# Optimization experiments

Measured on AMD Instinct MI355X. Metric: run time of the kernel, lower is better.

The kernel has to match this reference:

```python
import jax, jax.numpy as jnp
import numpy as np
from jax import lax

B, S, T, V, E, H = 32, 128, 64, 32000, 512, 512
STEPS = T - 1


def gru_cell(x, h, Wih, Whh, bih, bhh):
    # PyTorch GRU cell: gates ordered (r, z, n)
    gi = x @ Wih.T + bih            # [B, 3H]
    gh = h @ Whh.T + bhh            # [B, 3H]
    ir, iz, inn = jnp.split(gi, 3, axis=-1)
    hr, hz, hn = jnp.split(gh, 3, axis=-1)
    r = jax.nn.sigmoid(ir + hr)
    z = jax.nn.sigmoid(iz + hz)
    n = jnp.tanh(inn + r * hn)
    return (1.0 - z) * n + z * h


def setup_inputs() -> dict:
    key = jax.random.key(0)
    ks = jax.random.split(key, 16)
    w = lambda k, shape: (jax.random.normal(k, shape, dtype=jnp.float32) * 0.05)
    src = jax.random.randint(ks[0], (B, S), 1, V)
    src_lengths = jax.random.randint(ks[1], (B,), 1, S + 1)
    tgt = jax.random.randint(ks[2], (B, T), 1, V)
    return {
        'src': src, 'src_lengths': src_lengths, 'tgt': tgt,
        # encoder
        'emb_enc': w(ks[3], (V, E)).at[0].set(0.0),   # padding_idx=0
        'Wih_e': w(ks[4], (3 * H, E)),
        'Whh_e': w(ks[5], (3 * H, H)),
        'bih_e': jnp.zeros((3 * H,), jnp.float32),
        'bhh_e': jnp.zeros((3 * H,), jnp.float32),
        # decoder
        'emb_dec': w(ks[6], (V, E)).at[0].set(0.0),
        'Wih_d': w(ks[7], (3 * H, E + H)),
        'Whh_d': w(ks[8], (3 * H, H)),
        'bih_d': jnp.zeros((3 * H,), jnp.float32),
        'bhh_d': jnp.zeros((3 * H,), jnp.float32),
        'Wc': w(ks[9], (H, 2 * H)),
        'bc': jnp.zeros((H,), jnp.float32),
        'Wo': w(ks[10], (V, H)),
        'bo': jnp.zeros((V,), jnp.float32),
    }


def _forward(src, src_lengths, tgt, emb_enc, Wih_e, Whh_e, bih_e, bhh_e,
             emb_dec, Wih_d, Whh_d, bih_d, bhh_d, Wc, bc, Wo, bo):
    # ---- encoder (packed-sequence semantics: state frozen / outputs zero past length) ----
    x = emb_enc[src]                                   # [B, S, E]
    xs = jnp.swapaxes(x, 0, 1)                         # [S, B, E]
    valid = jnp.arange(S)[:, None] < src_lengths[None, :]  # [S, B]
    h0 = jnp.zeros((src.shape[0], H), x.dtype)

    def enc_step(h, inp):
        xt, vt = inp
        hn = gru_cell(xt, h, Wih_e, Whh_e, bih_e, bhh_e)
        h = jnp.where(vt[:, None], hn, h)
        out = jnp.where(vt[:, None], hn, 0.0)
        return h, out

    h_enc, enc_outs = lax.scan(enc_step, h0, (xs, valid))
    enc_outs = jnp.swapaxes(enc_outs, 0, 1)            # [B, S, H]
    mask = jnp.arange(S)[None, :] < src_lengths[:, None]  # [B, S]

    # ---- decoder loop (teacher forcing ratio 1.0 -> input = tgt[:, t]) ----
    tokens = jnp.swapaxes(tgt[:, :STEPS], 0, 1)        # [STEPS, B]

    def dec_step(h, tok):
        e = emb_dec[tok]                               # [B, E]
        query = h                                      # hidden[-1], 1 layer
        scores = jnp.einsum('bsh,bh->bs', enc_outs, query)
        scores = jnp.where(mask, scores, -jnp.inf)
        aw = jax.nn.softmax(scores, axis=1)            # [B, S]
        ctx = jnp.einsum('bs,bsh->bh', aw, enc_outs)   # [B, H]
        rnn_in = jnp.concatenate([e, ctx], axis=-1)    # [B, E+H]
        hn = gru_cell(rnn_in, h, Wih_d, Whh_d, bih_d, bhh_d)
        cc = jnp.tanh(jnp.concatenate([hn, ctx], axis=-1) @ Wc.T + bc)
        logits = cc @ Wo.T + bo                        # [B, V]
        return hn, (logits, aw)

    _, (logits, attns) = lax.scan(dec_step, h_enc, tokens)
    logits = jnp.swapaxes(logits, 0, 1)                # [B, STEPS, V]
    attns = jnp.swapaxes(attns, 0, 1)                  # [B, STEPS, S]
    return logits, attns


def reference(src, src_lengths, tgt, emb_enc, Wih_e, Whh_e, bih_e, bhh_e,
              emb_dec, Wih_d, Whh_d, bih_d, bhh_d, Wc, bc, Wo, bo):
    return _forward(src, src_lengths, tgt, emb_enc, Wih_e, Whh_e, bih_e, bhh_e,
                    emb_dec, Wih_d, Whh_d, bih_d, bhh_d, Wc, bc, Wo, bo)
```

## Files before the change

### kernel.cpp

```cpp
#include <hip/hip_runtime.h>
#include <hip/hip_fp16.h>
#include <cmath>

#define B_ 32
#define S_ 128
#define T_ 64
#define STEPS_ 63
#define V_ 32000
#define E_ 512
#define H_ 512

typedef __attribute__((ext_vector_type(4))) float f32x4;
typedef __attribute__((ext_vector_type(8))) short bf16x8;
typedef __attribute__((ext_vector_type(2))) _Float16 f16x2;

__device__ inline short f2bf(float x) {
  unsigned u = __builtin_bit_cast(unsigned, x);
  u = (u + 0x7fffu + ((u >> 16) & 1u)) >> 16;
  return (short)u;
}
__device__ inline float bf2f(short h) {
  unsigned u = ((unsigned)(unsigned short)h) << 16;
  return __builtin_bit_cast(float, u);
}
__device__ inline float fdot2(__half2 a, __half2 b, float c) {
#if __has_builtin(__builtin_amdgcn_fdot2)
  return __builtin_amdgcn_fdot2(__builtin_bit_cast(f16x2, a),
                                __builtin_bit_cast(f16x2, b), c, false);
#else
  float2 af = __half22float2(a), bf = __half22float2(b);
  return c + af.x * bf.x + af.y * bf.y;
#endif
}
__device__ inline float sigm(float x) { return 1.f / (1.f + expf(-x)); }

__global__ __launch_bounds__(256) void k_pack_w3(
    const float* __restrict__ W, int ldw, int col0, __half* __restrict__ W3) {
  int idx = blockIdx.x * 256 + threadIdx.x;
  int up = idx & 255, g = (idx >> 8) % 3, kq = idx / 768;
  const float* r0 = W + (long)(g * 512 + 2 * up) * ldw + col0 + 4 * kq;
  const float* r1 = r0 + ldw;
  __half h[8];
  h[0] = __float2half(r0[0]); h[1] = __float2half(r0[1]);
  h[2] = __float2half(r1[0]); h[3] = __float2half(r1[1]);
  h[4] = __float2half(r0[2]); h[5] = __float2half(r0[3]);
  h[6] = __float2half(r1[2]); h[7] = __float2half(r1[3]);
  *(uint4*)(W3 + (long)idx * 8) = *(uint4*)h;
}

__global__ __launch_bounds__(256) void k_mfma_gemm(
    const float* __restrict__ A, const float* __restrict__ emb,
    const int* __restrict__ tok, int amode,
    const float* __restrict__ Bmat, long ldb,
    const float* __restrict__ bias,
    void* __restrict__ outp, long sb, long st,
    int M, int N, int K, int outmode, int passes) {
  __shared__ short Ah[128 * 40];
  __shared__ short Al[128 * 40];
  __shared__ short Bh[128 * 40];
  __shared__ short Bl[128 * 40];
  int t = threadIdx.x;
  int n0 = blockIdx.x * 128, m0 = blockIdx.y * 128;
  int ar = t >> 2, ac = (t & 3) * 8;

  const float* arow0;
  const float* arow1;
  {
    int m = m0 + ar;       int mc = m < M ? m : M - 1;
    int m2 = m0 + ar + 64; int mc2 = m2 < M ? m2 : M - 1;
    if (amode == 0) {
      arow0 = A + (long)mc * K;
      arow1 = A + (long)mc2 * K;
    } else {
      int b = mc & 31, q = mc >> 5;
      int tk = (amode == 1) ? tok[b * S_ + q] : tok[b * T_ + q];
      arow0 = emb + (long)tk * K;
      b = mc2 & 31; q = mc2 >> 5;
      tk = (amode == 1) ? tok[b * S_ + q] : tok[b * T_ + q];
      arow1 = emb + (long)tk * K;
    }
  }
  const float* brow0 = Bmat + (long)(n0 + ar) * ldb;
  const float* brow1 = Bmat + (long)(n0 + ar + 64) * ldb;

  int lane = t & 63, wave = t >> 6;
  int wm = (wave >> 1) * 64, wn = (wave & 1) * 64;
  int lr = lane & 15, lk = lane >> 4;
  f32x4 acc[4][4] = {};

  for (int k0 = 0; k0 < K; k0 += 32) {
    auto stage = [&](const float* rowp, short* Dh, short* Dl, int r) {
      float4 x0 = *(const float4*)(rowp + k0 + ac);
      float4 x1 = *(const float4*)(rowp + k0 + ac + 4);
      float xs[8] = {x0.x, x0.y, x0.z, x0.w, x1.x, x1.y, x1.z, x1.w};
      bf16x8 hi, lo;
#pragma unroll
      for (int i = 0; i < 8; ++i) {
        short h = f2bf(xs[i]);
        hi[i] = h;
        lo[i] = f2bf(xs[i] - bf2f(h));
      }
      *(bf16x8*)&Dh[r * 40 + ac] = hi;
      if (passes > 1) *(bf16x8*)&Dl[r * 40 + ac] = lo;
    };
    stage(arow0, Ah, Al, ar);
    stage(arow1, Ah, Al, ar + 64);
    stage(brow0, Bh, Bl, ar);
    stage(brow1, Bh, Bl, ar + 64);
    __syncthreads();

    bf16x8 a_h[4], b_h[4];
#pragma unroll
    for (int i = 0; i < 4; ++i) {
      a_h[i] = *(const bf16x8*)&Ah[(wm + i * 16 + lr) * 40 + lk * 8];
      b_h[i] = *(const bf16x8*)&Bh[(wn + i * 16 + lr) * 40 + lk * 8];
    }
    if (passes > 1) {
      bf16x8 a_l[4], b_l[4];
#pragma unroll
      for (int i = 0; i < 4; ++i) {
        a_l[i] = *(const bf16x8*)&Al[(wm + i * 16 + lr) * 40 + lk * 8];
        b_l[i] = *(const bf16x8*)&Bl[(wn + i * 16 + lr) * 40 + lk * 8];
      }
#pragma unroll
      for (int i = 0; i < 4; ++i)
#pragma unroll
        for (int j = 0; j < 4; ++j) {
          acc[i][j] = __builtin_amdgcn_mfma_f32_16x16x32_bf16(a_l[i], b_h[j], acc[i][j], 0, 0, 0);
          acc[i][j] = __builtin_amdgcn_mfma_f32_16x16x32_bf16(a_h[i], b_l[j], acc[i][j], 0, 0, 0);
        }
    }
#pragma unroll
    for (int i = 0; i < 4; ++i)
#pragma unroll
      for (int j = 0; j < 4; ++j)
        acc[i][j] = __builtin_amdgcn_mfma_f32_16x16x32_bf16(a_h[i], b_h[j], acc[i][j], 0, 0, 0);
    __syncthreads();
  }

#pragma unroll
  for (int i = 0; i < 4; ++i) {
#pragma unroll
    for (int r = 0; r < 4; ++r) {
      int m = m0 + wm + i * 16 + lk * 4 + r;
      if (m >= M) continue;
      long base = (long)(m & 31) * sb + (long)(m >> 5) * st;
#pragma unroll
      for (int j = 0; j < 4; ++j) {
        int n = n0 + wn + j * 16 + lr;
        float v = acc[i][j][r] + bias[n];
        if (outmode == 2) ((__half*)outp)[base + n] = __float2half(v);
        else ((float*)outp)[base + n] = (outmode == 1) ? tanhf(v) : v;
      }
    }
  }
}

__global__ __launch_bounds__(1024) void k_enc_all(
    const float* __restrict__ gi_all,
    const __half* __restrict__ W3,
    const float* __restrict__ bhh, const int* __restrict__ lens,
    float* __restrict__ h_out,
    __half* __restrict__ EO16,
    float* __restrict__ EO32) {
  __shared__ __align__(8) __half2 hs16[256];
  __shared__ float pGh[1536];
  __shared__ float gis[1536];
  int b = blockIdx.x, t = threadIdx.x;
  int len = lens[b];
  float br0 = 0, br1 = 0, bz0 = 0, bz1 = 0, bn0 = 0, bn1 = 0, hold0 = 0, hold1 = 0;
  if (t < 256) {
    br0 = bhh[2 * t]; br1 = bhh[2 * t + 1];
    bz0 = bhh[512 + 2 * t]; bz1 = bhh[512 + 2 * t + 1];
    bn0 = bhh[1024 + 2 * t]; bn1 = bhh[1024 + 2 * t + 1];
    hs16[t] = __float22half2_rn(make_float2(0.f, 0.f));
  }
  __syncthreads();

  for (int s = 0; s < S_; ++s) {
    if (s == len) break;
    if (t >= 256) {
      int c = t - 256, g = c >> 8, up = c & 255;
      const __half* wb = W3 + (long)(g * 256 + up) * 8;
      float a0 = 0.f, a1 = 0.f;
#pragma unroll 8
      for (int kq = 0; kq < 128; ++kq) {
        uint4 w8 = *(const uint4*)(wb + (long)kq * 6144);
        const __half2* wp = (const __half2*)&w8;
        __half2 x01 = hs16[2 * kq], x23 = hs16[2 * kq + 1];
        a0 = fdot2(x01, wp[0], a0); a1 = fdot2(x01, wp[1], a1);
        a0 = fdot2(x23, wp[2], a0); a1 = fdot2(x23, wp[3], a1);
      }
      pGh[g * 512 + 2 * up] = a0;
      pGh[g * 512 + 2 * up + 1] = a1;
    } else {
      const float* gi = gi_all + ((long)s * 32 + b) * 1536;
      int i0 = t * 6;
#pragma unroll
      for (int i = 0; i < 6; ++i) gis[i0 + i] = gi[i0 + i];
    }
    __syncthreads();
    if (t < 256) {
      int u0 = 2 * t;
      float r0 = sigm(gis[u0] + pGh[u0] + br0);
      float r1 = sigm(gis[u0 + 1] + pGh[u0 + 1] + br1);
      float z0 = sigm(gis[512 + u0] + pGh[512 + u0] + bz0);
      float z1 = sigm(gis[512 + u0 + 1] + pGh[512 + u0 + 1] + bz1);
      float n0 = tanhf(gis[1024 + u0] + r0 * (pGh[1024 + u0] + bn0));
      float n1 = tanhf(gis[1024 + u0 + 1] + r1 * (pGh[1024 + u0 + 1] + bn1));
      hold0 = (1.f - z0) * n0 + z0 * hold0;
      hold1 = (1.f - z1) * n1 + z1 * hold1;
      __half2 h2 = __float22half2_rn(make_float2(hold0, hold1));
      hs16[t] = h2;
      long row = (long)b * 128 + s;
      *(__half2*)(EO16 + row * 512 + u0) = h2;
      *(float2*)(EO32 + row * 512 + u0) = make_float2(hold0, hold1);
    }
    __syncthreads();
  }
  if (t < 256) *(float2*)(h_out + b * 512 + 2 * t) = make_float2(hold0, hold1);
}

__global__ __launch_bounds__(1024) void k_dec_all(
    const float* __restrict__ gie,
    const __half* __restrict__ EO16g,
    const __half* __restrict__ W3,
    const __half* __restrict__ GV,
    const float* __restrict__ bhh, const int* __restrict__ lens,
    const float* __restrict__ h_init,
    float* __restrict__ hctx,
    float* __restrict__ attns) {
  __shared__ __align__(16) __half2 EOs[32768];
  __shared__ __align__(8) __half2 hs16[256];
  __shared__ float pGh[1536];
  __shared__ float pGc[1536];
  __shared__ float gis[1536];
  __shared__ float sc[128];
  __shared__ float wred[8];
  int b = blockIdx.x, t = threadIdx.x;
  int lane = t & 63, wave = t >> 6;
  int len = lens[b];
  float br0 = 0, br1 = 0, bz0 = 0, bz1 = 0, bn0 = 0, bn1 = 0, hold0 = 0, hold1 = 0;
  if (t < 256) {
    br0 = bhh[2 * t]; br1 = bhh[2 * t + 1];
    bz0 = bhh[512 + 2 * t]; bz1 = bhh[512 + 2 * t + 1];
    bn0 = bhh[1024 + 2 * t]; bn1 = bhh[1024 + 2 * t + 1];
    float2 h2 = *(const float2*)(h_init + b * 512 + 2 * t);
    hold0 = h2.x; hold1 = h2.y;
    hs16[t] = __float22half2_rn(h2);
  }
  {
    const uint4* src = (const uint4*)(EO16g + (long)b * 128 * 512);
    uint4* dst = (uint4*)EOs;
    for (int i = t; i < 8192; i += 1024) dst[i] = src[i];
  }
  __syncthreads();
  const __half2* GVb = (const __half2*)GV + (long)b * 128 * 768;

  for (int step = 0; step < STEPS_; ++step) {
    long row = (long)step * 32 + b;
    {
      uint4 hv = ((const uint4*)hs16)[lane];
      const __half2* hp = (const __half2*)&hv;
#pragma unroll
      for (int si = 0; si < 8; ++si) {
        int s = wave * 8 + si;
        uint4 ev = ((const uint4*)&EOs[s * 256])[lane];
        const __half2* ep = (const __half2*)&ev;
        float p = 0.f;
#pragma unroll
        for (int q = 0; q < 4; ++q) p = fdot2(ep[q], hp[q], p);
#pragma unroll
        for (int off = 32; off > 0; off >>= 1) p += __shfl_down(p, off, 64);
        if (lane == 0) sc[s] = p;
      }
    }
    __syncthreads();
    if (t < 128) {
      float v = (t < len) ? sc[t] : -INFINITY;
      float wm = v;
#pragma unroll
      for (int off = 32; off > 0; off >>= 1) wm = fmaxf(wm, __shfl_down(wm, off, 64));
      if (lane == 0) wred[wave] = wm;
    } else if (t < 512) {
      const float* gi = gie + row * 1536;
      int i0 = (t - 128) * 4;
      *(float4*)(gis + i0) = *(const float4*)(gi + i0);
    }
    __syncthreads();
    if (t < 128) {
      float m = fmaxf(wred[0], wred[1]);
      float e = (t < len) ? expf(sc[t] - m) : 0.f;
      float es = e;
#pragma unroll
      for (int off = 32; off > 0; off >>= 1) es += __shfl_down(es, off, 64);
      if (lane == 0) wred[4 + wave] = es;
      __syncthreads();
      float aw = e / (wred[4] + wred[5]);
      sc[t] = aw;
      attns[((long)b * STEPS_ + step) * 128 + t] = aw;
    } else {
      __syncthreads();
    }
    __syncthreads();
    if (t < 768) {
      int g = t >> 8, up = t & 255;
      const __half* wb = W3 + (long)(g * 256 + up) * 8;
      float a0 = 0.f, a1 = 0.f;
#pragma unroll 8
      for (int kq = 0; kq < 128; ++kq) {
        uint4 w8 = *(const uint4*)(wb + (long)kq * 6144);
        const __half2* wp = (const __half2*)&w8;
        __half2 x01 = hs16[2 * kq], x23 = hs16[2 * kq + 1];
        a0 = fdot2(x01, wp[0], a0); a1 = fdot2(x01, wp[1], a1);
        a0 = fdot2(x23, wp[2], a0); a1 = fdot2(x23, wp[3], a1);
      }
      pGh[g * 512 + 2 * up] = a0;
      pGh[g * 512 + 2 * up + 1] = a1;
    } else if (t < 960) {
      int c4 = (t - 768) * 4;
      float ax0 = 0, ay0 = 0, ax1 = 0, ay1 = 0, ax2 = 0, ay2 = 0, ax3 = 0, ay3 = 0;
#pragma unroll 2
      for (int s = 0; s < 128; ++s) {
        if (s == len) break;
        float aw = sc[s];
        uint4 g4 = *(const uint4*)(GVb + (long)s * 768 + c4);
        const __half2* gp = (const __half2*)&g4;
        float2 f0 = __half22float2(gp[0]), f1 = __half22float2(gp[1]);
        float2 f2 = __half22float2(gp[2]), f3 = __half22float2(gp[3]);
        ax0 += aw * f0.x; ay0 += aw * f0.y;
        ax1 += aw * f1.x; ay1 += aw * f1.y;
        ax2 += aw * f2.x; ay2 += aw * f2.y;
        ax3 += aw * f3.x; ay3 += aw * f3.y;
      }
      pGc[2 * c4 + 0] = ax0; pGc[2 * c4 + 1] = ay0;
      pGc[2 * c4 + 2] = ax1; pGc[2 * c4 + 3] = ay1;
      pGc[2 * c4 + 4] = ax2; pGc[2 * c4 + 5] = ay2;
      pGc[2 * c4 + 6] = ax3; pGc[2 * c4 + 7] = ay3;
    } else {
      int ec = (t - 960) * 4;
      float ax0 = 0, ay0 = 0, ax1 = 0, ay1 = 0, ax2 = 0, ay2 = 0, ax3 = 0, ay3 = 0;
#pragma unroll 2
      for (int s = 0; s < 128; ++s) {
        if (s == len) break;
        float aw = sc[s];
        uint4 e4 = ((const uint4*)&EOs[s * 256])[t - 960];
        const __half2* ep = (const __half2*)&e4;
        float2 f0 = __half22float2(ep[0]), f1 = __half22float2(ep[1]);
        float2 f2 = __half22float2(ep[2]), f3 = __half22float2(ep[3]);
        ax0 += aw * f0.x; ay0 += aw * f0.y;
        ax1 += aw * f1.x; ay1 += aw * f1.y;
        ax2 += aw * f2.x; ay2 += aw * f2.y;
        ax3 += aw * f3.x; ay3 += aw * f3.y;
      }
      float* crow = hctx + row * 1024 + 512 + 2 * ec;
      *(float2*)(crow + 0) = make_float2(ax0, ay0);
      *(float2*)(crow + 2) = make_float2(ax1, ay1);
      *(float2*)(crow + 4) = make_float2(ax2, ay2);
      *(float2*)(crow + 6) = make_float2(ax3, ay3);
    }
    __syncthreads();
    if (t < 256) {
      int u0 = 2 * t;
      float r0 = sigm(gis[u0] + pGc[u0] + pGh[u0] + br0);
      float r1 = sigm(gis[u0 + 1] + pGc[u0 + 1] + pGh[u0 + 1] + br1);
      float z0 = sigm(gis[512 + u0] + pGc[512 + u0] + pGh[512 + u0] + bz0);
      float z1 = sigm(gis[512 + u0 + 1] + pGc[512 + u0 + 1] + pGh[512 + u0 + 1] + bz1);
      float n0 = tanhf(gis[1024 + u0] + pGc[1024 + u0] + r0 * (pGh[1024 + u0] + bn0));
      float n1 = tanhf(gis[1024 + u0 + 1] + pGc[1024 + u0 + 1] + r1 * (pGh[1024 + u0 + 1] + bn1));
      hold0 = (1.f - z0) * n0 + z0 * hold0;
      hold1 = (1.f - z1) * n1 + z1 * hold1;
      hs16[t] = __float22half2_rn(make_float2(hold0, hold1));
      *(float2*)(hctx + row * 1024 + u0) = make_float2(hold0, hold1);
    }
    __syncthreads();
  }
}

extern "C" void kernel_launch(void* const* d_in, const int* in_sizes, int n_in,
                              void* d_out, int out_size, void* d_ws, size_t ws_size,
                              hipStream_t stream) {
  (void)in_sizes; (void)n_in; (void)out_size; (void)ws_size;
  const int*   src   = (const int*)d_in[0];
  const int*   lens  = (const int*)d_in[1];
  const int*   tgt   = (const int*)d_in[2];
  const float* emb_e = (const float*)d_in[3];
  const float* Wih_e = (const float*)d_in[4];
  const float* Whh_e = (const float*)d_in[5];
  const float* bih_e = (const float*)d_in[6];
  const float* bhh_e = (const float*)d_in[7];
  const float* emb_d = (const float*)d_in[8];
  const float* Wih_d = (const float*)d_in[9];
  const float* Whh_d = (const float*)d_in[10];
  const float* bih_d = (const float*)d_in[11];
  const float* bhh_d = (const float*)d_in[12];
  const float* Wc    = (const float*)d_in[13];
  const float* bc    = (const float*)d_in[14];
  const float* Wo    = (const float*)d_in[15];
  const float* bo    = (const float*)d_in[16];

  float* logits = (float*)d_out;
  float* attns  = (float*)d_out + (long)B_ * STEPS_ * V_;

  float* w = (float*)d_ws;
  __half* W3e  = (__half*)w;
  __half* W3d  = (__half*)(w + 393216);
  float*  zb   = w + 786432;
  float*  GIe  = w + 788480;
  float*  GId  = GIe + 6291456;
  __half* EO16 = (__half*)(GId + 3145728);
  float*  EO32 = GId + 3145728 + 1048576;
  float*  h0   = EO32 + 2097152;
  __half* GV    = (__half*)GIe;
  float*  hctx  = GIe + 3145728;
  float*  ccall = GIe + 5242880;

  hipMemsetAsync(EO16, 0, 2097152 * sizeof(__half), stream);
  hipMemsetAsync(EO32, 0, 2097152 * sizeof(float), stream);
  hipMemsetAsync(zb, 0, 1536 * sizeof(float), stream);

  k_pack_w3<<<384, 256, 0, stream>>>(Whh_e, 512, 0, W3e);
  k_pack_w3<<<384, 256, 0, stream>>>(Whh_d, 512, 0, W3d);

  k_mfma_gemm<<<dim3(1536 / 128, 4096 / 128), 256, 0, stream>>>(
      nullptr, emb_e, src, 1, Wih_e, 512, bih_e, GIe, 1536L, 32L * 1536L,
      4096, 1536, 512, 0, 1);
  k_mfma_gemm<<<dim3(1536 / 128, (2016 + 127) / 128), 256, 0, stream>>>(
      nullptr, emb_d, tgt, 2, Wih_d, 1024, bih_d, GId, 1536L, 32L * 1536L,
      2016, 1536, 512, 0, 1);

  k_enc_all<<<32, 1024, 0, stream>>>(GIe, W3e, bhh_e, lens, h0, EO16, EO32);

  k_mfma_gemm<<<dim3(1536 / 128, 4096 / 128), 256, 0, stream>>>(
      EO32, nullptr, nullptr, 0, Wih_d + 512, 1024, zb, GV, 1536L, 49152L,
      4096, 1536, 512, 2, 3);

  k_dec_all<<<32, 1024, 0, stream>>>(GId, EO16, W3d, GV, bhh_d, lens, h0,
                                     hctx, attns);

  k_mfma_gemm<<<dim3(512 / 128, (2016 + 127) / 128), 256, 0, stream>>>(
      hctx, nullptr, nullptr, 0, Wc, 1024, bc, ccall, 512L, 16384L,
      2016, 512, 1024, 1, 3);

  k_mfma_gemm<<<dim3(V_ / 128, (2016 + 127) / 128), 256, 0, stream>>>(
      ccall, nullptr, nullptr, 0, Wo, 512, bo, logits,
      (long)STEPS_ * V_, (long)V_, 2016, 32000, 512, 0, 3);
}
```

Measured before the change: 3.426 ms.

## Keep recurrent Whh weights resident in registers across encoder and decoder steps

Repacks Whh so that each of the 1024 threads preloads 96 uint4 (all three gates for one hidden unit over half of K) into registers once, instead of re-reading the packed weights from global/L2 every time step. All threads now take part in the h@Whh matvec, with a pair shuffle to combine the two K halves, and the separate pGh shared buffer and one barrier per step are removed. The decoder softmax is collapsed into a single wave, and the context accumulation is split across more threads with narrower per-thread work. This needs about 384 VGPRs per thread for weights, so there is risk of spilling or of the register limit under launch_bounds(1024,4).

```diff
diff --git a/kernel.cpp b/kernel.cpp
--- a/kernel.cpp
+++ b/kernel.cpp
@@ -34,18 +34,16 @@
 }
 __device__ inline float sigm(float x) { return 1.f / (1.f + expf(-x)); }
 
-__global__ __launch_bounds__(256) void k_pack_w3(
-    const float* __restrict__ W, int ldw, int col0, __half* __restrict__ W3) {
+__global__ __launch_bounds__(256) void k_pack_w4(
+    const float* __restrict__ W, int ldw, int col0, uint4* __restrict__ W4) {
   int idx = blockIdx.x * 256 + threadIdx.x;
-  int up = idx & 255, g = (idx >> 8) % 3, kq = idx / 768;
-  const float* r0 = W + (long)(g * 512 + 2 * up) * ldw + col0 + 4 * kq;
-  const float* r1 = r0 + ldw;
+  int t = idx & 1023, i = idx >> 10;
+  int g = i >> 5, ii = i & 31, u = t >> 1, kh = t & 1;
+  const float* r = W + (long)(g * 512 + u) * ldw + col0 + kh * 256 + ii * 8;
   __half h[8];
-  h[0] = __float2half(r0[0]); h[1] = __float2half(r0[1]);
-  h[2] = __float2half(r1[0]); h[3] = __float2half(r1[1]);
-  h[4] = __float2half(r0[2]); h[5] = __float2half(r0[3]);
-  h[6] = __float2half(r1[2]); h[7] = __float2half(r1[3]);
-  *(uint4*)(W3 + (long)idx * 8) = *(uint4*)h;
+#pragma unroll
+  for (int j = 0; j < 8; ++j) h[j] = __float2half(r[j]);
+  W4[idx] = *(uint4*)h;
 }
 
 __global__ __launch_bounds__(256) void k_mfma_gemm(
@@ -156,98 +154,94 @@
   }
 }
 
-__global__ __launch_bounds__(1024) void k_enc_all(
+__global__ __launch_bounds__(1024, 4) void k_enc_all(
     const float* __restrict__ gi_all,
-    const __half* __restrict__ W3,
+    const uint4* __restrict__ W4,
     const float* __restrict__ bhh, const int* __restrict__ lens,
     float* __restrict__ h_out,
     __half* __restrict__ EO16,
     float* __restrict__ EO32) {
-  __shared__ __align__(8) __half2 hs16[256];
-  __shared__ float pGh[1536];
-  __shared__ float gis[1536];
+  __shared__ __align__(16) __half hs16[512];
   int b = blockIdx.x, t = threadIdx.x;
+  int u = t >> 1, kh = t & 1;
   int len = lens[b];
-  float br0 = 0, br1 = 0, bz0 = 0, bz1 = 0, bn0 = 0, bn1 = 0, hold0 = 0, hold1 = 0;
-  if (t < 256) {
-    br0 = bhh[2 * t]; br1 = bhh[2 * t + 1];
-    bz0 = bhh[512 + 2 * t]; bz1 = bhh[512 + 2 * t + 1];
-    bn0 = bhh[1024 + 2 * t]; bn1 = bhh[1024 + 2 * t + 1];
-    hs16[t] = __float22half2_rn(make_float2(0.f, 0.f));
-  }
+  uint4 wreg[96];
+#pragma unroll
+  for (int i = 0; i < 96; ++i) wreg[i] = W4[(long)i * 1024 + t];
+  float bhr = bhh[u], bhz = bhh[512 + u], bhn = bhh[1024 + u];
+  float hcur = 0.f;
+  if (kh == 0) hs16[u] = __float2half(0.f);
   __syncthreads();
 
   for (int s = 0; s < S_; ++s) {
     if (s == len) break;
-    if (t >= 256) {
-      int c = t - 256, g = c >> 8, up = c & 255;
-      const __half* wb = W3 + (long)(g * 256 + up) * 8;
-      float a0 = 0.f, a1 = 0.f;
-#pragma unroll 8
-      for (int kq = 0; kq < 128; ++kq) {
-        uint4 w8 = *(const uint4*)(wb + (long)kq * 6144);
-        const __half2* wp = (const __half2*)&w8;
-        __half2 x01 = hs16[2 * kq], x23 = hs16[2 * kq + 1];
-        a0 = fdot2(x01, wp[0], a0); a1 = fdot2(x01, wp[1], a1);
-        a0 = fdot2(x23, wp[2], a0); a1 = fdot2(x23, wp[3], a1);
-      }
-      pGh[g * 512 + 2 * up] = a0;
-      pGh[g * 512 + 2 * up + 1] = a1;
-    } else {
+    float gi_r = 0, gi_z = 0, gi_n = 0;
+    if (kh == 0) {
       const float* gi = gi_all + ((long)s * 32 + b) * 1536;
-      int i0 = t * 6;
-#pragma unroll
-      for (int i = 0; i < 6; ++i) gis[i0 + i] = gi[i0 + i];
-    }
-    __syncthreads();
-    if (t < 256) {
-      int u0 = 2 * t;
-      float r0 = sigm(gis[u0] + pGh[u0] + br0);
-      float r1 = sigm(gis[u0 + 1] + pGh[u0 + 1] + br1);
-      float z0 = sigm(gis[512 + u0] + pGh[512 + u0] + bz0);
-      float z1 = sigm(gis[512 + u0 + 1] + pGh[512 + u0 + 1] + bz1);
-      float n0 = tanhf(gis[1024 + u0] + r0 * (pGh[1024 + u0] + bn0));
-      float n1 = tanhf(gis[1024 + u0 + 1] + r1 * (pGh[1024 + u0 + 1] + bn1));
-      hold0 = (1.f - z0) * n0 + z0 * hold0;
-      hold1 = (1.f - z1) * n1 + z1 * hold1;
-      __half2 h2 = __float22half2_rn(make_float2(hold0, hold1));
-      hs16[t] = h2;
+      gi_r = gi[u]; gi_z = gi[512 + u]; gi_n = gi[1024 + u];
+    }
+    float ar = 0.f, az = 0.f, an = 0.f;
+    const uint4* xv4 = ((const uint4*)hs16) + kh * 32;
+#pragma unroll
+    for (int i = 0; i < 32; ++i) {
+      uint4 xv = xv4[i];
+      const __half2* xp = (const __half2*)&xv;
+      const __half2* wr = (const __half2*)&wreg[i];
+      const __half2* wz = (const __half2*)&wreg[32 + i];
+      const __half2* wn = (const __half2*)&wreg[64 + i];
+#pragma unroll
+      for (int q = 0; q < 4; ++q) {
+        ar = fdot2(xp[q], wr[q], ar);
+        az = fdot2(xp[q], wz[q], az);
+        an = fdot2(xp[q], wn[q], an);
+      }
+    }
+    ar += __shfl_xor(ar, 1, 64);
+    az += __shfl_xor(az, 1, 64);
+    an += __shfl_xor(an, 1, 64);
+    __syncthreads();
+    if (kh == 0) {
+      float r = sigm(gi_r + ar + bhr);
+      float z = sigm(gi_z + az + bhz);
+      float n = tanhf(gi_n + r * (an + bhn));
+      hcur = (1.f - z) * n + z * hcur;
+      __half hh = __float2half(hcur);
+      hs16[u] = hh;
       long row = (long)b * 128 + s;
-      *(__half2*)(EO16 + row * 512 + u0) = h2;
-      *(float2*)(EO32 + row * 512 + u0) = make_float2(hold0, hold1);
-    }
-    __syncthreads();
-  }
-  if (t < 256) *(float2*)(h_out + b * 512 + 2 * t) = make_float2(hold0, hold1);
-}
-
-__global__ __launch_bounds__(1024) void k_dec_all(
+      EO16[row * 512 + u] = hh;
+      EO32[row * 512 + u] = hcur;
+    }
+    __syncthreads();
+  }
+  if (kh == 0) h_out[b * 512 + u] = hcur;
+}
+
+__global__ __launch_bounds__(1024, 4) void k_dec_all(
     const float* __restrict__ gie,
     const __half* __restrict__ EO16g,
-    const __half* __restrict__ W3,
+    const uint4* __restrict__ W4,
     const __half* __restrict__ GV,
     const float* __restrict__ bhh, const int* __restrict__ lens,
     const float* __restrict__ h_init,
     float* __restrict__ hctx,
     float* __restrict__ attns) {
   __shared__ __align__(16) __half2 EOs[32768];
-  __shared__ __align__(8) __half2 hs16[256];
-  __shared__ float pGh[1536];
+  __shared__ __align__(16) __half hs16[512];
   __shared__ float pGc[1536];
   __shared__ float gis[1536];
   __shared__ float sc[128];
-  __shared__ float wred[8];
   int b = blockIdx.x, t = threadIdx.x;
   int lane = t & 63, wave = t >> 6;
+  int u = t >> 1, kh = t & 1;
   int len = lens[b];
-  float br0 = 0, br1 = 0, bz0 = 0, bz1 = 0, bn0 = 0, bn1 = 0, hold0 = 0, hold1 = 0;
-  if (t < 256) {
-    br0 = bhh[2 * t]; br1 = bhh[2 * t + 1];
-    bz0 = bhh[512 + 2 * t]; bz1 = bhh[512 + 2 * t + 1];
-    bn0 = bhh[1024 + 2 * t]; bn1 = bhh[1024 + 2 * t + 1];
-    float2 h2 = *(const float2*)(h_init + b * 512 + 2 * t);
-    hold0 = h2.x; hold1 = h2.y;
-    hs16[t] = __float22half2_rn(h2);
+  uint4 wreg[96];
+#pragma unroll
+  for (int i = 0; i < 96; ++i) wreg[i] = W4[(long)i * 1024 + t];
+  float bhr = bhh[u], bhz = bhh[512 + u], bhn = bhh[1024 + u];
+  float hcur = 0.f;
+  if (kh == 0) {
+    hcur = h_init[b * 512 + u];
+    hs16[u] = __float2half(hcur);
   }
   {
     const uint4* src = (const uint4*)(EO16g + (long)b * 128 * 512);
@@ -276,102 +270,81 @@
       }
     }
     __syncthreads();
-    if (t < 128) {
-      float v = (t < len) ? sc[t] : -INFINITY;
-      float wm = v;
-#pragma unroll
-      for (int off = 32; off > 0; off >>= 1) wm = fmaxf(wm, __shfl_down(wm, off, 64));
-      if (lane == 0) wred[wave] = wm;
-    } else if (t < 512) {
-      const float* gi = gie + row * 1536;
-      int i0 = (t - 128) * 4;
-      *(float4*)(gis + i0) = *(const float4*)(gi + i0);
-    }
-    __syncthreads();
-    if (t < 128) {
-      float m = fmaxf(wred[0], wred[1]);
-      float e = (t < len) ? expf(sc[t] - m) : 0.f;
-      float es = e;
-#pragma unroll
-      for (int off = 32; off > 0; off >>= 1) es += __shfl_down(es, off, 64);
-      if (lane == 0) wred[4 + wave] = es;
-      __syncthreads();
-      float aw = e / (wred[4] + wred[5]);
-      sc[t] = aw;
-      attns[((long)b * STEPS_ + step) * 128 + t] = aw;
-    } else {
-      __syncthreads();
+    if (t < 64) {
+      float p0 = sc[lane], p1 = sc[64 + lane];
+      bool v0 = lane < len, v1 = 64 + lane < len;
+      float m = fmaxf(v0 ? p0 : -INFINITY, v1 ? p1 : -INFINITY);
+#pragma unroll
+      for (int off = 32; off > 0; off >>= 1) m = fmaxf(m, __shfl_xor(m, off, 64));
+      float e0 = v0 ? expf(p0 - m) : 0.f;
+      float e1 = v1 ? expf(p1 - m) : 0.f;
+      float S = e0 + e1;
+#pragma unroll
+      for (int off = 32; off > 0; off >>= 1) S += __shfl_xor(S, off, 64);
+      float aw0 = e0 / S, aw1 = e1 / S;
+      sc[lane] = aw0;
+      sc[64 + lane] = aw1;
+      float* ap = attns + ((long)b * STEPS_ + step) * 128;
+      ap[lane] = aw0;
+      ap[64 + lane] = aw1;
+    } else if (t < 448) {
+      int i0 = (t - 64) * 4;
+      *(float4*)(gis + i0) = *(const float4*)(gie + row * 1536 + i0);
     }
     __syncthreads();
     if (t < 768) {
-      int g = t >> 8, up = t & 255;
-      const __half* wb = W3 + (long)(g * 256 + up) * 8;
-      float a0 = 0.f, a1 = 0.f;
-#pragma unroll 8
-      for (int kq = 0; kq < 128; ++kq) {
-        uint4 w8 = *(const uint4*)(wb + (long)kq * 6144);
-        const __half2* wp = (const __half2*)&w8;
-        __half2 x01 = hs16[2 * kq], x23 = hs16[2 * kq + 1];
-        a0 = fdot2(x01, wp[0], a0); a1 = fdot2(x01, wp[1], a1);
-        a0 = fdot2(x23, wp[2], a0); a1 = fdot2(x23, wp[3], a1);
-      }
-      pGh[g * 512 + 2 * up] = a0;
-      pGh[g * 512 + 2 * up + 1] = a1;
-    } else if (t < 960) {
-      int c4 = (t - 768) * 4;
-      float ax0 = 0, ay0 = 0, ax1 = 0, ay1 = 0, ax2 = 0, ay2 = 0, ax3 = 0, ay3 = 0;
-#pragma unroll 2
+      float ax = 0.f, ay = 0.f;
       for (int s = 0; s < 128; ++s) {
         if (s == len) break;
         float aw = sc[s];
-        uint4 g4 = *(const uint4*)(GVb + (long)s * 768 + c4);
-        const __half2* gp = (const __half2*)&g4;
-        float2 f0 = __half22float2(gp[0]), f1 = __half22float2(gp[1]);
-        float2 f2 = __half22float2(gp[2]), f3 = __half22float2(gp[3]);
-        ax0 += aw * f0.x; ay0 += aw * f0.y;
-        ax1 += aw * f1.x; ay1 += aw * f1.y;
-        ax2 += aw * f2.x; ay2 += aw * f2.y;
-        ax3 += aw * f3.x; ay3 += aw * f3.y;
-      }
-      pGc[2 * c4 + 0] = ax0; pGc[2 * c4 + 1] = ay0;
-      pGc[2 * c4 + 2] = ax1; pGc[2 * c4 + 3] = ay1;
-      pGc[2 * c4 + 4] = ax2; pGc[2 * c4 + 5] = ay2;
-      pGc[2 * c4 + 6] = ax3; pGc[2 * c4 + 7] = ay3;
+        float2 g2 = __half22float2(GVb[(long)s * 768 + t]);
+        ax += aw * g2.x;
+        ay += aw * g2.y;
+      }
+      pGc[2 * t] = ax;
+      pGc[2 * t + 1] = ay;
     } else {
-      int ec = (t - 960) * 4;
-      float ax0 = 0, ay0 = 0, ax1 = 0, ay1 = 0, ax2 = 0, ay2 = 0, ax3 = 0, ay3 = 0;
-#pragma unroll 2
+      int c = t - 768;
+      float ax = 0.f, ay = 0.f;
       for (int s = 0; s < 128; ++s) {
         if (s == len) break;
         float aw = sc[s];
-        uint4 e4 = ((const uint4*)&EOs[s * 256])[t - 960];
-        const __half2* ep = (const __half2*)&e4;
-        float2 f0 = __half22float2(ep[0]), f1 = __half22float2(ep[1]);
-        float2 f2 = __half22float2(ep[2]), f3 = __half22float2(ep[3]);
-        ax0 += aw * f0.x; ay0 += aw * f0.y;
-        ax1 += aw * f1.x; ay1 += aw * f1.y;
-        ax2 += aw * f2.x; ay2 += aw * f2.y;
-        ax3 += aw * f3.x; ay3 += aw * f3.y;
-      }
-      float* crow = hctx + row * 1024 + 512 + 2 * ec;
-      *(float2*)(crow + 0) = make_float2(ax0, ay0);
-      *(float2*)(crow + 2) = make_float2(ax1, ay1);
-      *(float2*)(crow + 4) = make_float2(ax2, ay2);
-      *(float2*)(crow + 6) = make_float2(ax3, ay3);
-    }
-    __syncthreads();
-    if (t < 256) {
-      int u0 = 2 * t;
-      float r0 = sigm(gis[u0] + pGc[u0] + pGh[u0] + br0);
-      float r1 = sigm(gis[u0 + 1] + pGc[u0 + 1] + pGh[u0 + 1] + br1);
-      float z0 = sigm(gis[512 + u0] + pGc[512 + u0] + pGh[512 + u0] + bz0);
-      float z1 = sigm(gis[512 + u0 + 1] + pGc[512 + u0 + 1] + pGh[512 + u0 + 1] + bz1);
-      float n0 = tanhf(gis[1024 + u0] + pGc[1024 + u0] + r0 * (pGh[1024 + u0] + bn0));
-      float n1 = tanhf(gis[1024 + u0 + 1] + pGc[1024 + u0 + 1] + r1 * (pGh[1024 + u0 + 1] + bn1));
-      hold0 = (1.f - z0) * n0 + z0 * hold0;
-      hold1 = (1.f - z1) * n1 + z1 * hold1;
-      hs16[t] = __float22half2_rn(make_float2(hold0, hold1));
-      *(float2*)(hctx + row * 1024 + u0) = make_float2(hold0, hold1);
+        float2 e2 = __half22float2(EOs[s * 256 + c]);
+        ax += aw * e2.x;
+        ay += aw * e2.y;
+      }
+      *(float2*)(hctx + row * 1024 + 512 + 2 * c) = make_float2(ax, ay);
+    }
+    __syncthreads();
+    float ar = 0.f, az = 0.f, an = 0.f;
+    {
+      const uint4* xv4 = ((const uint4*)hs16) + kh * 32;
+#pragma unroll
+      for (int i = 0; i < 32; ++i) {
+        uint4 xv = xv4[i];
+        const __half2* xp = (const __half2*)&xv;
+        const __half2* wr = (const __half2*)&wreg[i];
+        const __half2* wz = (const __half2*)&wreg[32 + i];
+        const __half2* wn = (const __half2*)&wreg[64 + i];
+#pragma unroll
+        for (int q = 0; q < 4; ++q) {
+          ar = fdot2(xp[q], wr[q], ar);
+          az = fdot2(xp[q], wz[q], az);
+          an = fdot2(xp[q], wn[q], an);
+        }
+      }
+      ar += __shfl_xor(ar, 1, 64);
+      az += __shfl_xor(az, 1, 64);
+      an += __shfl_xor(an, 1, 64);
+    }
+    __syncthreads();
+    if (kh == 0) {
+      float r = sigm(gis[u] + pGc[u] + ar + bhr);
+      float z = sigm(gis[512 + u] + pGc[512 + u] + az + bhz);
+      float n = tanhf(gis[1024 + u] + pGc[1024 + u] + r * (an + bhn));
+      hcur = (1.f - z) * n + z * hcur;
+      hs16[u] = __float2half(hcur);
+      hctx[row * 1024 + u] = hcur;
     }
     __syncthreads();
   }
@@ -403,8 +376,8 @@
   float* attns  = (float*)d_out + (long)B_ * STEPS_ * V_;
 
   float* w = (float*)d_ws;
-  __half* W3e  = (__half*)w;
-  __half* W3d  = (__half*)(w + 393216);
+  uint4*  W4e  = (uint4*)w;
+  uint4*  W4d  = (uint4*)(w + 393216);
   float*  zb   = w + 786432;
   float*  GIe  = w + 788480;
   float*  GId  = GIe + 6291456;
@@ -419,8 +392,8 @@
   hipMemsetAsync(EO32, 0, 2097152 * sizeof(float), stream);
   hipMemsetAsync(zb, 0, 1536 * sizeof(float), stream);
 
-  k_pack_w3<<<384, 256, 0, stream>>>(Whh_e, 512, 0, W3e);
-  k_pack_w3<<<384, 256, 0, stream>>>(Whh_d, 512, 0, W3d);
+  k_pack_w4<<<384, 256, 0, stream>>>(Whh_e, 512, 0, W4e);
+  k_pack_w4<<<384, 256, 0, stream>>>(Whh_d, 512, 0, W4d);
 
   k_mfma_gemm<<<dim3(1536 / 128, 4096 / 128), 256, 0, stream>>>(
       nullptr, emb_e, src, 1, Wih_e, 512, bih_e, GIe, 1536L, 32L * 1536L,
@@ -429,13 +402,13 @@
       nullptr, emb_d, tgt, 2, Wih_d, 1024, bih_d, GId, 1536L, 32L * 1536L,
       2016, 1536, 512, 0, 1);
 
-  k_enc_all<<<32, 1024, 0, stream>>>(GIe, W3e, bhh_e, lens, h0, EO16, EO32);
+  k_enc_all<<<32, 1024, 0, stream>>>(GIe, W4e, bhh_e, lens, h0, EO16, EO32);
 
   k_mfma_gemm<<<dim3(1536 / 128, 4096 / 128), 256, 0, stream>>>(
       EO32, nullptr, nullptr, 0, Wih_d + 512, 1024, zb, GV, 1536L, 49152L,
       4096, 1536, 512, 2, 3);
 
-  k_dec_all<<<32, 1024, 0, stream>>>(GId, EO16, W3d, GV, bhh_d, lens, h0,
+  k_dec_all<<<32, 1024, 0, stream>>>(GId, EO16, W4d, GV, bhh_d, lens, h0,
                                      hctx, attns);
 
   k_mfma_gemm<<<dim3(512 / 128, (2016 + 127) / 128), 256, 0, stream>>>(
```

New measurement: 9.115 ms. 166% more time.

## Overlap attention scores with hidden matvec and fold softmax into one wave

Applied to the files above, without the earlier changes.

Each decoder step previously ran attention scoring on all 16 waves, then the W_hh matvec. Now the 12 matvec waves run concurrently with 4 waves computing the 128 attention scores. The softmax is done by a single wave using xor-shuffle reductions, which removes several block barriers per step. The context and GV accumulations are re-split so each thread handles one half2 instead of four. The last mfma_gemm argument also changes from 3 to 1 in three GEMM launches, likely a precision or mode switch. The narrower per-thread accumulation loops have less instruction-level parallelism and a longer serial chain.

```diff
diff --git a/kernel.cpp b/kernel.cpp
--- a/kernel.cpp
+++ b/kernel.cpp
@@ -32,6 +32,7 @@
   return c + af.x * bf.x + af.y * bf.y;
 #endif
 }
+__device__ inline __half2 bc2(unsigned v) { return __builtin_bit_cast(__half2, v); }
 __device__ inline float sigm(float x) { return 1.f / (1.f + expf(-x)); }
 
 __global__ __launch_bounds__(256) void k_pack_w3(
@@ -186,10 +187,9 @@
 #pragma unroll 8
       for (int kq = 0; kq < 128; ++kq) {
         uint4 w8 = *(const uint4*)(wb + (long)kq * 6144);
-        const __half2* wp = (const __half2*)&w8;
         __half2 x01 = hs16[2 * kq], x23 = hs16[2 * kq + 1];
-        a0 = fdot2(x01, wp[0], a0); a1 = fdot2(x01, wp[1], a1);
-        a0 = fdot2(x23, wp[2], a0); a1 = fdot2(x23, wp[3], a1);
+        a0 = fdot2(x01, bc2(w8.x), a0); a1 = fdot2(x01, bc2(w8.y), a1);
+        a0 = fdot2(x23, bc2(w8.z), a0); a1 = fdot2(x23, bc2(w8.w), a1);
       }
       pGh[g * 512 + 2 * up] = a0;
       pGh[g * 512 + 2 * up + 1] = a1;
@@ -236,7 +236,6 @@
   __shared__ float pGc[1536];
   __shared__ float gis[1536];
   __shared__ float sc[128];
-  __shared__ float wred[8];
   int b = blockIdx.x, t = threadIdx.x;
   int lane = t & 63, wave = t >> 6;
   int len = lens[b];
@@ -259,50 +258,6 @@
 
   for (int step = 0; step < STEPS_; ++step) {
     long row = (long)step * 32 + b;
-    {
-      uint4 hv = ((const uint4*)hs16)[lane];
-      const __half2* hp = (const __half2*)&hv;
-#pragma unroll
-      for (int si = 0; si < 8; ++si) {
-        int s = wave * 8 + si;
-        uint4 ev = ((const uint4*)&EOs[s * 256])[lane];
-        const __half2* ep = (const __half2*)&ev;
-        float p = 0.f;
-#pragma unroll
-        for (int q = 0; q < 4; ++q) p = fdot2(ep[q], hp[q], p);
-#pragma unroll
-        for (int off = 32; off > 0; off >>= 1) p += __shfl_down(p, off, 64);
-        if (lane == 0) sc[s] = p;
-      }
-    }
-    __syncthreads();
-    if (t < 128) {
-      float v = (t < len) ? sc[t] : -INFINITY;
-      float wm = v;
-#pragma unroll
-      for (int off = 32; off > 0; off >>= 1) wm = fmaxf(wm, __shfl_down(wm, off, 64));
-      if (lane == 0) wred[wave] = wm;
-    } else if (t < 512) {
-      const float* gi = gie + row * 1536;
-      int i0 = (t - 128) * 4;
-      *(float4*)(gis + i0) = *(const float4*)(gi + i0);
-    }
-    __syncthreads();
-    if (t < 128) {
-      float m = fmaxf(wred[0], wred[1]);
-      float e = (t < len) ? expf(sc[t] - m) : 0.f;
-      float es = e;
-#pragma unroll
-      for (int off = 32; off > 0; off >>= 1) es += __shfl_down(es, off, 64);
-      if (lane == 0) wred[4 + wave] = es;
-      __syncthreads();
-      float aw = e / (wred[4] + wred[5]);
-      sc[t] = aw;
-      attns[((long)b * STEPS_ + step) * 128 + t] = aw;
-    } else {
-      __syncthreads();
-    }
-    __syncthreads();
     if (t < 768) {
       int g = t >> 8, up = t & 255;
       const __half* wb = W3 + (long)(g * 256 + up) * 8;
@@ -310,54 +265,75 @@
 #pragma unroll 8
       for (int kq = 0; kq < 128; ++kq) {
         uint4 w8 = *(const uint4*)(wb + (long)kq * 6144);
-        const __half2* wp = (const __half2*)&w8;
         __half2 x01 = hs16[2 * kq], x23 = hs16[2 * kq + 1];
-        a0 = fdot2(x01, wp[0], a0); a1 = fdot2(x01, wp[1], a1);
-        a0 = fdot2(x23, wp[2], a0); a1 = fdot2(x23, wp[3], a1);
+        a0 = fdot2(x01, bc2(w8.x), a0); a1 = fdot2(x01, bc2(w8.y), a1);
+        a0 = fdot2(x23, bc2(w8.z), a0); a1 = fdot2(x23, bc2(w8.w), a1);
       }
       pGh[g * 512 + 2 * up] = a0;
       pGh[g * 512 + 2 * up + 1] = a1;
-    } else if (t < 960) {
-      int c4 = (t - 768) * 4;
-      float ax0 = 0, ay0 = 0, ax1 = 0, ay1 = 0, ax2 = 0, ay2 = 0, ax3 = 0, ay3 = 0;
-#pragma unroll 2
+    } else {
+      int w = wave - 12;
+      uint4 hv = ((const uint4*)hs16)[lane];
+      __half2 h0 = bc2(hv.x), h1 = bc2(hv.y), h2 = bc2(hv.z), h3 = bc2(hv.w);
+#pragma unroll 4
+      for (int si = 0; si < 32; ++si) {
+        int s = w * 32 + si;
+        uint4 ev = ((const uint4*)&EOs[s * 256])[lane];
+        float p = 0.f;
+        p = fdot2(bc2(ev.x), h0, p);
+        p = fdot2(bc2(ev.y), h1, p);
+        p = fdot2(bc2(ev.z), h2, p);
+        p = fdot2(bc2(ev.w), h3, p);
+#pragma unroll
+        for (int off = 32; off > 0; off >>= 1) p += __shfl_down(p, off, 64);
+        if (lane == 0) sc[s] = p;
+      }
+    }
+    __syncthreads();
+    if (t < 64) {
+      float p0 = sc[lane], p1 = sc[64 + lane];
+      bool v0 = lane < len, v1 = 64 + lane < len;
+      float m = fmaxf(v0 ? p0 : -INFINITY, v1 ? p1 : -INFINITY);
+#pragma unroll
+      for (int off = 32; off > 0; off >>= 1) m = fmaxf(m, __shfl_xor(m, off, 64));
+      float e0 = v0 ? expf(p0 - m) : 0.f;
+      float e1 = v1 ? expf(p1 - m) : 0.f;
+      float S = e0 + e1;
+#pragma unroll
+      for (int off = 32; off > 0; off >>= 1) S += __shfl_xor(S, off, 64);
+      float aw0 = e0 / S, aw1 = e1 / S;
+      sc[lane] = aw0;
+      sc[64 + lane] = aw1;
+      float* ap = attns + ((long)b * STEPS_ + step) * 128;
+      ap[lane] = aw0;
+      ap[64 + lane] = aw1;
+    } else if (t < 448) {
+      int i0 = (t - 64) * 4;
+      *(float4*)(gis + i0) = *(const float4*)(gie + row * 1536 + i0);
+    }
+    __syncthreads();
+    if (t < 768) {
+      float ax = 0.f, ay = 0.f;
       for (int s = 0; s < 128; ++s) {
         if (s == len) break;
         float aw = sc[s];
-        uint4 g4 = *(const uint4*)(GVb + (long)s * 768 + c4);
-        const __half2* gp = (const __half2*)&g4;
-        float2 f0 = __half22float2(gp[0]), f1 = __half22float2(gp[1]);
-        float2 f2 = __half22float2(gp[2]), f3 = __half22float2(gp[3]);
-        ax0 += aw * f0.x; ay0 += aw * f0.y;
-        ax1 += aw * f1.x; ay1 += aw * f1.y;
-        ax2 += aw * f2.x; ay2 += aw * f2.y;
-        ax3 += aw * f3.x; ay3 += aw * f3.y;
-      }
-      pGc[2 * c4 + 0] = ax0; pGc[2 * c4 + 1] = ay0;
-      pGc[2 * c4 + 2] = ax1; pGc[2 * c4 + 3] = ay1;
-      pGc[2 * c4 + 4] = ax2; pGc[2 * c4 + 5] = ay2;
-      pGc[2 * c4 + 6] = ax3; pGc[2 * c4 + 7] = ay3;
+        float2 g2 = __half22float2(GVb[(long)s * 768 + t]);
+        ax += aw * g2.x;
+        ay += aw * g2.y;
+      }
+      pGc[2 * t] = ax;
+      pGc[2 * t + 1] = ay;
     } else {
-      int ec = (t - 960) * 4;
-      float ax0 = 0, ay0 = 0, ax1 = 0, ay1 = 0, ax2 = 0, ay2 = 0, ax3 = 0, ay3 = 0;
-#pragma unroll 2
+      int c = t - 768;
+      float ax = 0.f, ay = 0.f;
       for (int s = 0; s < 128; ++s) {
         if (s == len) break;
         float aw = sc[s];
-        uint4 e4 = ((const uint4*)&EOs[s * 256])[t - 960];
-        const __half2* ep = (const __half2*)&e4;
-        float2 f0 = __half22float2(ep[0]), f1 = __half22float2(ep[1]);
-        float2 f2 = __half22float2(ep[2]), f3 = __half22float2(ep[3]);
-        ax0 += aw * f0.x; ay0 += aw * f0.y;
-        ax1 += aw * f1.x; ay1 += aw * f1.y;
-        ax2 += aw * f2.x; ay2 += aw * f2.y;
-        ax3 += aw * f3.x; ay3 += aw * f3.y;
-      }
-      float* crow = hctx + row * 1024 + 512 + 2 * ec;
-      *(float2*)(crow + 0) = make_float2(ax0, ay0);
-      *(float2*)(crow + 2) = make_float2(ax1, ay1);
-      *(float2*)(crow + 4) = make_float2(ax2, ay2);
-      *(float2*)(crow + 6) = make_float2(ax3, ay3);
+        float2 e2 = __half22float2(EOs[s * 256 + c]);
+        ax += aw * e2.x;
+        ay += aw * e2.y;
+      }
+      *(float2*)(hctx + row * 1024 + 512 + 2 * c) = make_float2(ax, ay);
     }
     __syncthreads();
     if (t < 256) {
@@ -433,16 +409,16 @@
 
   k_mfma_gemm<<<dim3(1536 / 128, 4096 / 128), 256, 0, stream>>>(
       EO32, nullptr, nullptr, 0, Wih_d + 512, 1024, zb, GV, 1536L, 49152L,
-      4096, 1536, 512, 2, 3);
+      4096, 1536, 512, 2, 1);
 
   k_dec_all<<<32, 1024, 0, stream>>>(GId, EO16, W3d, GV, bhh_d, lens, h0,
                                      hctx, attns);
 
   k_mfma_gemm<<<dim3(512 / 128, (2016 + 127) / 128), 256, 0, stream>>>(
       hctx, nullptr, nullptr, 0, Wc, 1024, bc, ccall, 512L, 16384L,
-      2016, 512, 1024, 1, 3);
+      2016, 512, 1024, 1, 1);
 
   k_mfma_gemm<<<dim3(V_ / 128, (2016 + 127) / 128), 256, 0, stream>>>(
       ccall, nullptr, nullptr, 0, Wo, 512, bo, logits,
-      (long)STEPS_ * V_, (long)V_, 2016, 32000, 512, 0, 3);
-}
+      (long)STEPS_ * V_, (long)V_, 2016, 32000, 512, 0, 1);
+}
```

Result: faster. 2.976 ms (-13.1%).
